# Optimization experiments

Hardware: AMD Instinct MI355X
Metric: run time of the kernel (lower is better)

## Reference

```python
import math
import jax, jax.numpy as jnp
import numpy as np
from jax import lax

LEAKY_SLOPE = 0.2
ACT_GAIN = math.sqrt(2.0)

def bilinear_filter():
    h = jnp.array([1.0, 3.0, 3.0, 1.0], dtype=jnp.float32)
    h = h[:, None] * h[None, :]
    return h / jnp.sum(h)

def setup_inputs() -> dict:
    key = jax.random.key(0)
    ks = jax.random.split(key, 6)
    B, Cin, Cout, W_DIM, R = 16, 512, 512, 512, 64
    return {
        "x": jax.random.normal(ks[0], (B, Cin, R // 2, R // 2), dtype=jnp.float32),
        "w": jax.random.normal(ks[1], (B, W_DIM), dtype=jnp.float32),
        "noise_raw": jax.random.normal(ks[2], (B, 1, R, R), dtype=jnp.float32),
        "affine_weight": jax.random.normal(ks[3], (Cin, W_DIM), dtype=jnp.float32),
        "affine_bias": jnp.ones((Cin,), dtype=jnp.float32),
        "weight": jax.random.normal(ks[4], (Cout, Cin, 3, 3), dtype=jnp.float32),
        "bias": 0.1 * jax.random.normal(ks[5], (Cout,), dtype=jnp.float32),
        "noise_strength": jnp.float32(1.0),
    }

def reference(x, w, noise_raw, affine_weight, affine_bias, weight, bias, noise_strength):
    B, Cin = x.shape[0], x.shape[1]
    Cout = weight.shape[0]
    w_dim = affine_weight.shape[1]
    # EqualizedLinear affine: weight_gain = 1/sqrt(in), bias_gain = 1, no activation
    styles = w @ (affine_weight * (1.0 / math.sqrt(w_dim))).T + affine_bias  # [B, Cin]
    # demodulation coefficients from modulated weights
    wmod = weight[None] * styles[:, None, :, None, None]                      # [B,Cout,Cin,3,3]
    dcoefs = lax.rsqrt(jnp.sum(jnp.square(wmod), axis=(2, 3, 4)) + 1e-8)     # [B, Cout]
    # modulate input instead of weights
    xs = x * styles[:, :, None, None]
    # up=True path: conv_transpose2d(x, weight.transpose(0,1), stride=2, padding=0)
    # == dilated conv with spatially flipped kernel, pad k-1=2
    w_flip = weight[:, :, ::-1, ::-1]
    y = lax.conv_general_dilated(
        xs, w_flip, window_strides=(1, 1), padding=[(2, 2), (2, 2)],
        lhs_dilation=(2, 2), dimension_numbers=("NCHW", "OIHW", "NCHW"))    # [B,Cout,2H+1,2H+1]
    # filter2d with 4x4 bilinear kernel, gain=4, padding=1 (depthwise)
    f = bilinear_filter() * 4.0
    kd = jnp.tile(f[None, None], (Cout, 1, 1, 1))                            # [Cout,1,4,4]
    y = lax.conv_general_dilated(
        y, kd, window_strides=(1, 1), padding=[(1, 1), (1, 1)],
        dimension_numbers=("NCHW", "OIHW", "NCHW"), feature_group_count=Cout)  # [B,Cout,2H,2H]
    # addcmul: noise + y * dcoefs
    noise = noise_raw * noise_strength
    y = noise + y * dcoefs[:, :, None, None]
    # bias, act gain sqrt(2), leaky relu 0.2
    y = (y + bias[None, :, None, None]) * ACT_GAIN
    return jnp.where(y >= 0, y, LEAKY_SLOPE * y)
```

## Files before the change

### kernel.cpp

```cpp
#include <hip/hip_runtime.h>
#include <hip/hip_bf16.h>
#include <stdint.h>

typedef float f32x4 __attribute__((ext_vector_type(4)));
typedef __bf16 bf16x8 __attribute__((ext_vector_type(8)));

#define GLDS16(gp, lp) __builtin_amdgcn_global_load_lds( \
    (const __attribute__((address_space(1))) void*)(gp), \
    (__attribute__((address_space(3))) void*)(lp), 16, 0, 0)

static __device__ __forceinline__ unsigned short f2bf(float f) {
    unsigned int u = __float_as_uint(f);
    u = (u + 0x7fffu + ((u >> 16) & 1u)) >> 16;
    return (unsigned short)u;
}
static __device__ __forceinline__ float bf2f(unsigned short v) {
    return __uint_as_float(((unsigned int)v) << 16);
}

#define O_STYLES 0
#define O_DCOEF  32768
#define O_XS     65536
#define O_WP     19005440
#define O_Y1     23724032
#define O_WSQ    23724032
#define WS_NEED  96075776
#define SP 1104

__global__ __launch_bounds__(256) void k_prepA(const float* __restrict__ w,
                                               const float* __restrict__ aw,
                                               const float* __restrict__ ab,
                                               const float* __restrict__ weight,
                                               float* __restrict__ styles,
                                               float* __restrict__ wsq,
                                               unsigned short* __restrict__ wp) {
    int bid = blockIdx.x;
    if (bid < 32) {
        int g = bid * 256 + threadIdx.x;
        int b = g >> 9, ci = g & 511;
        const float4* wr = (const float4*)(w + b * 512);
        const float4* ar = (const float4*)(aw + ci * 512);
        float acc = 0.f;
        for (int k = 0; k < 128; ++k) {
            float4 wv = wr[k], av = ar[k];
            acc += wv.x * av.x + wv.y * av.y + wv.z * av.z + wv.w * av.w;
        }
        styles[g] = acc * 0.04419417382415922f + ab[ci];
    } else {
        int g = (bid - 32) * 256 + threadIdx.x;
        const float* wb = weight + (long)g * 9;
        float v[9]; float s = 0.f;
#pragma unroll
        for (int t = 0; t < 9; ++t) { v[t] = wb[t]; s += v[t] * v[t]; }
        wsq[g] = s;
        const int wri[9] = {2, 2, 0, 0, 2, 0, 1, 1, 1};
        const int wci[9] = {2, 0, 2, 0, 1, 1, 2, 0, 1};
#pragma unroll
        for (int t = 0; t < 9; ++t)
            wp[t * 262144 + g] = f2bf(v[wri[t] * 3 + wci[t]]);
    }
}

__global__ __launch_bounds__(256) void k_prepB(const float* __restrict__ styles,
                                               const float* __restrict__ wsq,
                                               const float* __restrict__ x,
                                               float* __restrict__ dcoefs,
                                               unsigned short* __restrict__ xs) {
    __shared__ float T[128][33];
    int bid = blockIdx.x;
    int t = threadIdx.x;
    if (bid < 32) {
        int g = bid * 256 + t;
        int b = g >> 9, co = g & 511;
        const float4* sr = (const float4*)(styles + b * 512);
        const float4* qr = (const float4*)(wsq + co * 512);
        float acc = 1e-8f;
        for (int k = 0; k < 128; ++k) {
            float4 sv = sr[k], qv = qr[k];
            acc += sv.x * sv.x * qv.x + sv.y * sv.y * qv.y + sv.z * sv.z * qv.z + sv.w * sv.w * qv.w;
        }
        dcoefs[g] = rsqrtf(acc);
        return;
    }
    int xb = bid - 32;
    int cc = xb & 3, i = (xb >> 2) & 31, b = xb >> 7;
    int ci0 = cc * 128;
    int j4 = (t & 7) * 4, cl_r = t >> 3;
    const float* xp = x + (((long)(b * 512 + ci0)) * 32 + i) * 32;
#pragma unroll
    for (int it = 0; it < 4; ++it) {
        int cl = cl_r + it * 32;
        float4 v = *(const float4*)(xp + cl * 1024 + j4);
        T[cl][j4] = v.x; T[cl][j4 + 1] = v.y; T[cl][j4 + 2] = v.z; T[cl][j4 + 3] = v.w;
    }
    __syncthreads();
    int ci_w = t & 127, jg = t >> 7;
    float sv = styles[b * 512 + ci0 + ci_w];
    unsigned short* op = xs + (((long)(b * 34 + (i + 1))) * 34 + 1) * 512 + ci0 + ci_w;
#pragma unroll
    for (int jj = 0; jj < 16; ++jj) {
        int j = jg * 16 + jj;
        op[(long)j * 512] = f2bf(T[ci_w][j] * sv);
    }
}

#define ST_A(kk) { GLDS16(xsB + sA0 + akt + (kk)*64, smp + nb + (kk)*16384 + t16); \
                   GLDS16(xsB + sA1 + akt + (kk)*64, smp + nb + (kk)*16384 + t16 + 8192); }
#define ST_B(kk) { GLDS16(wpB + sB0 + bkt + (kk)*64, smp + nb + 32768 + (kk)*16384 + t16); \
                   GLDS16(wpB + sB1 + bkt + (kk)*64, smp + nb + 32768 + (kk)*16384 + t16 + 8192); }
#define PHASE2(kk, STG, TAILBAR) { \
  _Pragma("unroll") for (int i = 0; i < 8; ++i) \
    av[i] = *(const bf16x8*)(smp + cb + (kk)*16384 + abase + (i*16)*64); \
  _Pragma("unroll") for (int j = 0; j < 4; ++j) \
    bv[j] = *(const bf16x8*)(smp + cb + (kk)*16384 + bbase + (j*16)*64); \
  STG; \
  __builtin_amdgcn_sched_barrier(0); \
  asm volatile("s_waitcnt vmcnt(4)" ::: "memory"); \
  __builtin_amdgcn_s_barrier(); \
  asm volatile("s_waitcnt lgkmcnt(0)" ::: "memory"); \
  __builtin_amdgcn_sched_barrier(0); \
  __builtin_amdgcn_s_setprio(1); \
  _Pragma("unroll") for (int i = 0; i < 8; ++i) \
    _Pragma("unroll") for (int j = 0; j < 4; ++j) \
      acc[i][j] = __builtin_amdgcn_mfma_f32_16x16x32_bf16(av[i], bv[j], acc[i][j], 0, 0, 0); \
  __builtin_amdgcn_s_setprio(0); \
  if (TAILBAR) __builtin_amdgcn_s_barrier(); }

__global__ __launch_bounds__(512, 2) void k_conv(const unsigned short* __restrict__ xs,
                                                 const unsigned short* __restrict__ wp,
                                                 unsigned short* __restrict__ y1) {
    extern __shared__ __align__(16) char smem[];
    const unsigned char* xsB = (const unsigned char*)xs;
    const unsigned char* wpB = (const unsigned char*)wp;
    char* smp = smem;

    int d = blockIdx.x;
    int pr, nt;
    if (d >= 544) { int r = d - 544; pr = 272 + (r & 3); nt = r >> 2; }
    else          { pr = (d >> 4) * 8 + (d & 7); nt = (d >> 3) & 1; }
    int par = pr / 69;
    int Mtile = pr - par * 69;
    int Ntile = nt;
    int a_par = par >> 1, c_par = par & 1;
    int ntaps = a_par ? (c_par ? 1 : 2) : (c_par ? 2 : 4);
    int tapofs = (par == 0) ? 0 : ((par == 1) ? 4 : ((par == 2) ? 6 : 8));
    int NKT = ntaps << 3;

    int tid = threadIdx.x;
    int lane = tid & 63, wave = tid >> 6;
    int wm = wave >> 2, wn = wave & 3;
    int lrow = lane & 15;
    int rchunk = (((lane >> 4) ^ ((lrow >> 1) & 3)) << 4);
    int abase = (wm * 128 + lrow) * 64 + rchunk;
    int bbase = 32768 + (wn * 64 + lrow) * 64 + rchunk;

    int srow = tid >> 2;
    int schunk = (((tid & 3) ^ ((tid >> 3) & 3)) << 4);
    int sA0, sA1;
    {
        unsigned gm = (unsigned)(Mtile * 256 + srow);
        if (gm > 17471u) gm = 17471u;
        unsigned b_ = gm / 1092u; unsigned pix = gm - b_ * 1092u;
        unsigned r = pix / 33u; unsigned s = pix - r * 33u;
        sA0 = (int)(((b_ * 34u + r) * 34u + s) << 10) + schunk;
        gm = (unsigned)(Mtile * 256 + srow + 128);
        if (gm > 17471u) gm = 17471u;
        b_ = gm / 1092u; pix = gm - b_ * 1092u;
        r = pix / 33u; s = pix - r * 33u;
        sA1 = (int)(((b_ * 34u + r) * 34u + s) << 10) + schunk;
    }
    int sB0 = ((Ntile * 256 + srow) << 10) + schunk;
    int sB1 = sB0 + (128 << 10);
    int t16 = tid << 4;

    f32x4 acc[8][4];
#pragma unroll
    for (int i = 0; i < 8; ++i)
#pragma unroll
        for (int j = 0; j < 4; ++j)
            acc[i][j] = (f32x4){0.f, 0.f, 0.f, 0.f};
    bf16x8 av[8], bv[4];

    auto mkA = [&](int kt) -> int {
        int tl = kt >> 3; if (tl >= ntaps) tl = ntaps - 1;
        int cib = kt & 7;
        int dio = a_par ? 1 : (c_par ? tl : (tl >> 1));
        int djo = c_par ? 1 : (a_par ? tl : (tl & 1));
        return dio * 34816 + djo * 1024 + cib * 128;
    };
    auto mkB = [&](int kt) -> long {
        int tl = kt >> 3; if (tl >= ntaps) tl = ntaps - 1;
        return (long)(tapofs + tl) * 524288 + (long)((kt & 7) * 128);
    };

    {
        int akt = mkA(0); long bkt = mkB(0); int nb = 0;
        ST_A(0); ST_B(0); ST_A(1); ST_B(1);
    }
    __builtin_amdgcn_sched_barrier(0);
    asm volatile("s_waitcnt vmcnt(4)" ::: "memory");
    __builtin_amdgcn_s_barrier();

    int cur = 0;
    for (int kt = 0; kt < NKT; ++kt) {
        int akt = mkA(kt + 1);
        long bkt = mkB(kt + 1);
        int nb = (cur ^ 1) << 16;
        int cb = cur << 16;
        PHASE2(0, { ST_A(0); ST_B(0); }, 0)
        PHASE2(1, { ST_A(1); ST_B(1); }, 1)
        cur ^= 1;
    }

#pragma unroll
    for (int mf = 0; mf < 8; ++mf) {
        int gm0 = Mtile * 256 + wm * 128 + mf * 16 + ((lane >> 4) << 2);
        if (gm0 < 17472) {
            unsigned ug = (unsigned)gm0;
            unsigned bb = ug / 1092u;
            int pix0 = (int)(ug - bb * 1092u);
            long rowb = ((long)((bb * 4u + par) * 512)) * SP;
#pragma unroll
            for (int nf = 0; nf < 4; ++nf) {
                int co = Ntile * 256 + wn * 64 + nf * 16 + lrow;
                unsigned short* dst = y1 + rowb + (long)co * SP + pix0;
                if (pix0 <= 1084) {
                    ushort4 pk;
                    pk.x = f2bf(acc[mf][nf][0]);
                    pk.y = f2bf(acc[mf][nf][1]);
                    pk.z = f2bf(acc[mf][nf][2]);
                    pk.w = f2bf(acc[mf][nf][3]);
                    *(ushort4*)dst = pk;
                } else if (pix0 == 1088) {
                    dst[0] = f2bf(acc[mf][nf][0]);
                }
            }
        }
    }
}

__global__ __launch_bounds__(256) void k_blur(const unsigned short* __restrict__ y1,
                                              const float* __restrict__ dcoefs,
                                              const float* __restrict__ bias,
                                              const float* __restrict__ noise,
                                              const float* __restrict__ nstr,
                                              float* __restrict__ out) {
    __shared__ float yl[4 * 1092];
    int bid = blockIdx.x;
    int cg = bid & 127, b = bid >> 7;
    int t = threadIdx.x;
    int n = t & 63, mq = t >> 6;
    float ns = nstr[0];

    const float* npb = noise + b * 4096;

    int o = n & 1;
    int se = n >> 1;
    int sp_ = se - 1 + o;
    float a0 = o ? 1.f : 3.f;
    float a1 = o ? 3.f : 1.f;

    for (int cc = 0; cc < 4; ++cc) {
        int co = cg * 4 + cc;
#pragma unroll
        for (int pl = 0; pl < 4; ++pl) {
            const unsigned short* src = y1 + ((long)((b * 4 + pl) * 512 + co)) * SP;
            float* dst = yl + pl * 1092;
            for (int it = t; it < 273; it += 256) {
                int p0 = it * 4;
                ushort4 v = *(const ushort4*)(src + p0);
                f32x4 fv;
                fv[0] = bf2f(v.x); fv[1] = bf2f(v.y);
                fv[2] = bf2f(v.z); fv[3] = bf2f(v.w);
                *(f32x4*)(dst + p0) = fv;
            }
        }
        __syncthreads();

        float dc = dcoefs[b * 512 + co];
        float bi = bias[co];
        float* ob = out + ((long)(b * 512 + co)) * 4096;

        auto H = [&](int ap, int r) -> float {
            if ((unsigned)r > 32u) return 0.f;
            const float* pe = yl + (ap * 2) * 1092 + r * 33;
            const float* po = pe + 1092;
            float pov = (sp_ >= 0) ? po[sp_] : 0.f;
            return a0 * pe[se] + a1 * pe[se + 1] + a1 * pov + a0 * po[sp_ + 1];
        };

        int m0 = mq * 16;
        int re = m0 >> 1;
        float he0 = H(0, re), he1 = H(0, re + 1);
        float ho0 = H(1, re - 1), ho1 = H(1, re);
#pragma unroll
        for (int k = 0; k < 16; k += 2) {
            int m = m0 + k;
            float ve = 3.f * he0 + he1 + ho0 + 3.f * ho1;
            float val = npb[m * 64 + n] * ns + ve * (0.0625f * dc);
            val = (val + bi) * 1.41421356237309515f;
            ob[m * 64 + n] = (val >= 0.f) ? val : 0.2f * val;
            float hn_o = H(1, re + 1);
            float vo = he0 + 3.f * he1 + 3.f * ho1 + hn_o;
            val = npb[(m + 1) * 64 + n] * ns + vo * (0.0625f * dc);
            val = (val + bi) * 1.41421356237309515f;
            ob[(m + 1) * 64 + n] = (val >= 0.f) ? val : 0.2f * val;
            ho0 = ho1; ho1 = hn_o;
            float hn_e = H(0, re + 2);
            he0 = he1; he1 = hn_e;
            re += 1;
        }
        __syncthreads();
    }
}

extern "C" void kernel_launch(void* const* d_in, const int* in_sizes, int n_in,
                              void* d_out, int out_size, void* d_ws, size_t ws_size,
                              hipStream_t stream) {
    (void)in_sizes; (void)n_in; (void)out_size;
    if (ws_size < (size_t)WS_NEED) return;
    const float* x      = (const float*)d_in[0];
    const float* w      = (const float*)d_in[1];
    const float* noise  = (const float*)d_in[2];
    const float* aw     = (const float*)d_in[3];
    const float* ab     = (const float*)d_in[4];
    const float* weight = (const float*)d_in[5];
    const float* bias   = (const float*)d_in[6];
    const float* nstr   = (const float*)d_in[7];
    float* out = (float*)d_out;
    char* ws = (char*)d_ws;
    float* styles          = (float*)(ws + O_STYLES);
    float* dcoefs          = (float*)(ws + O_DCOEF);
    unsigned short* xs     = (unsigned short*)(ws + O_XS);
    unsigned short* wp     = (unsigned short*)(ws + O_WP);
    unsigned short* y1     = (unsigned short*)(ws + O_Y1);
    float* wsq             = (float*)(ws + O_WSQ);

    hipFuncSetAttribute((const void*)k_conv,
                        hipFuncAttributeMaxDynamicSharedMemorySize, 131072);

    hipMemsetAsync(xs, 0, 18939904, stream);
    k_prepA<<<1056, 256, 0, stream>>>(w, aw, ab, weight, styles, wsq, wp);
    k_prepB<<<2080, 256, 0, stream>>>(styles, wsq, x, dcoefs, xs);
    k_conv <<<552,  512, 131072, stream>>>(xs, wp, y1);
    k_blur <<<2048, 256, 0, stream>>>(y1, dcoefs, bias, noise, nstr, out);
}
```

Measured before the change: 192.3 us.

## Shrink conv GEMM tiles to 128x128 with 256 threads and zero only padding borders

The implicit-GEMM conv kernel moves from 256x256 tiles with 512 threads and 128KB LDS to 128x128 tiles with 256 threads and 64KB LDS. That raises the grid from 552 to 2192 blocks, which should spread work more evenly across CUs and cut the tail-wave imbalance. The full memset of the padded xs buffer is replaced by extra prepA blocks that zero only the border rows and columns, saving write bandwidth. The smaller tiles trade away operand reuse per block, so global and LDS traffic per FLOP goes up.

```diff
diff --git a/kernel.cpp b/kernel.cpp
--- a/kernel.cpp
+++ b/kernel.cpp
@@ -33,10 +33,12 @@
                                                const float* __restrict__ weight,
                                                float* __restrict__ styles,
                                                float* __restrict__ wsq,
-                                               unsigned short* __restrict__ wp) {
+                                               unsigned short* __restrict__ wp,
+                                               unsigned short* __restrict__ xs) {
     int bid = blockIdx.x;
+    int t = threadIdx.x;
     if (bid < 32) {
-        int g = bid * 256 + threadIdx.x;
+        int g = bid * 256 + t;
         int b = g >> 9, ci = g & 511;
         const float4* wr = (const float4*)(w + b * 512);
         const float4* ar = (const float4*)(aw + ci * 512);
@@ -46,18 +48,31 @@
             acc += wv.x * av.x + wv.y * av.y + wv.z * av.z + wv.w * av.w;
         }
         styles[g] = acc * 0.04419417382415922f + ab[ci];
-    } else {
-        int g = (bid - 32) * 256 + threadIdx.x;
+    } else if (bid < 1056) {
+        int g = (bid - 32) * 256 + t;
         const float* wb = weight + (long)g * 9;
         float v[9]; float s = 0.f;
 #pragma unroll
-        for (int t = 0; t < 9; ++t) { v[t] = wb[t]; s += v[t] * v[t]; }
+        for (int q = 0; q < 9; ++q) { v[q] = wb[q]; s += v[q] * v[q]; }
         wsq[g] = s;
         const int wri[9] = {2, 2, 0, 0, 2, 0, 1, 1, 1};
         const int wci[9] = {2, 0, 2, 0, 1, 1, 2, 0, 1};
 #pragma unroll
-        for (int t = 0; t < 9; ++t)
-            wp[t * 262144 + g] = f2bf(v[wri[t] * 3 + wci[t]]);
+        for (int q = 0; q < 9; ++q)
+            wp[q * 262144 + g] = f2bf(v[wri[q] * 3 + wci[q]]);
+    } else {
+        int b = bid - 1056;
+        for (int it = 0; it < 66; ++it) {
+            int idx = t + it * 256;
+            int pos = idx >> 7, q = idx & 127;
+            int r, c;
+            if (pos < 34)       { r = 0;         c = pos; }
+            else if (pos < 68)  { r = 33;        c = pos - 34; }
+            else if (pos < 100) { r = pos - 67;  c = 0; }
+            else                { r = pos - 99;  c = 33; }
+            ushort4 z = {0, 0, 0, 0};
+            *(ushort4*)(xs + (((long)(b * 34 + r)) * 34 + c) * 512 + q * 4) = z;
+        }
     }
 }
 
@@ -104,15 +119,15 @@
     }
 }
 
-#define ST_A(kk) { GLDS16(xsB + sA0 + akt + (kk)*64, smp + nb + (kk)*16384 + t16); \
-                   GLDS16(xsB + sA1 + akt + (kk)*64, smp + nb + (kk)*16384 + t16 + 8192); }
-#define ST_B(kk) { GLDS16(wpB + sB0 + bkt + (kk)*64, smp + nb + 32768 + (kk)*16384 + t16); \
-                   GLDS16(wpB + sB1 + bkt + (kk)*64, smp + nb + 32768 + (kk)*16384 + t16 + 8192); }
+#define ST_A(kk) { GLDS16(xsB + sA0 + akt + (kk)*64, smp + nb + (kk)*8192 + t16); \
+                   GLDS16(xsB + sA1 + akt + (kk)*64, smp + nb + (kk)*8192 + t16 + 4096); }
+#define ST_B(kk) { GLDS16(wpB + sB0 + bkt + (kk)*64, smp + nb + 16384 + (kk)*8192 + t16); \
+                   GLDS16(wpB + sB1 + bkt + (kk)*64, smp + nb + 16384 + (kk)*8192 + t16 + 4096); }
 #define PHASE2(kk, STG, TAILBAR) { \
-  _Pragma("unroll") for (int i = 0; i < 8; ++i) \
-    av[i] = *(const bf16x8*)(smp + cb + (kk)*16384 + abase + (i*16)*64); \
+  _Pragma("unroll") for (int i = 0; i < 4; ++i) \
+    av[i] = *(const bf16x8*)(smp + cb + (kk)*8192 + abase + (i*16)*64); \
   _Pragma("unroll") for (int j = 0; j < 4; ++j) \
-    bv[j] = *(const bf16x8*)(smp + cb + (kk)*16384 + bbase + (j*16)*64); \
+    bv[j] = *(const bf16x8*)(smp + cb + 16384 + (kk)*8192 + bbase + (j*16)*64); \
   STG; \
   __builtin_amdgcn_sched_barrier(0); \
   asm volatile("s_waitcnt vmcnt(4)" ::: "memory"); \
@@ -120,27 +135,27 @@
   asm volatile("s_waitcnt lgkmcnt(0)" ::: "memory"); \
   __builtin_amdgcn_sched_barrier(0); \
   __builtin_amdgcn_s_setprio(1); \
-  _Pragma("unroll") for (int i = 0; i < 8; ++i) \
+  _Pragma("unroll") for (int i = 0; i < 4; ++i) \
     _Pragma("unroll") for (int j = 0; j < 4; ++j) \
       acc[i][j] = __builtin_amdgcn_mfma_f32_16x16x32_bf16(av[i], bv[j], acc[i][j], 0, 0, 0); \
   __builtin_amdgcn_s_setprio(0); \
   if (TAILBAR) __builtin_amdgcn_s_barrier(); }
 
-__global__ __launch_bounds__(512, 2) void k_conv(const unsigned short* __restrict__ xs,
-                                                 const unsigned short* __restrict__ wp,
-                                                 unsigned short* __restrict__ y1) {
+__global__ __launch_bounds__(256) void k_conv(const unsigned short* __restrict__ xs,
+                                              const unsigned short* __restrict__ wp,
+                                              unsigned short* __restrict__ y1) {
     extern __shared__ __align__(16) char smem[];
     const unsigned char* xsB = (const unsigned char*)xs;
     const unsigned char* wpB = (const unsigned char*)wp;
     char* smp = smem;
 
     int d = blockIdx.x;
-    int pr, nt;
-    if (d >= 544) { int r = d - 544; pr = 272 + (r & 3); nt = r >> 2; }
-    else          { pr = (d >> 4) * 8 + (d & 7); nt = (d >> 3) & 1; }
-    int par = pr / 69;
-    int Mtile = pr - par * 69;
-    int Ntile = nt;
+    int j, nt2;
+    if (d < 2176) { int g = d >> 5, r = d & 31; j = g * 8 + (r & 7); nt2 = r >> 3; }
+    else          { int r = d - 2176; j = 544 + (r & 3); nt2 = r >> 2; }
+    int par = j / 137;
+    int Mtile = j - par * 137;
+    int Ntile = nt2;
     int a_par = par >> 1, c_par = par & 1;
     int ntaps = a_par ? (c_par ? 1 : 2) : (c_par ? 2 : 4);
     int tapofs = (par == 0) ? 0 : ((par == 1) ? 4 : ((par == 2) ? 6 : 8));
@@ -148,38 +163,38 @@
 
     int tid = threadIdx.x;
     int lane = tid & 63, wave = tid >> 6;
-    int wm = wave >> 2, wn = wave & 3;
+    int wm = wave >> 1, wn = wave & 1;
     int lrow = lane & 15;
     int rchunk = (((lane >> 4) ^ ((lrow >> 1) & 3)) << 4);
-    int abase = (wm * 128 + lrow) * 64 + rchunk;
-    int bbase = 32768 + (wn * 64 + lrow) * 64 + rchunk;
+    int abase = (wm * 64 + lrow) * 64 + rchunk;
+    int bbase = (wn * 64 + lrow) * 64 + rchunk;
 
     int srow = tid >> 2;
     int schunk = (((tid & 3) ^ ((tid >> 3) & 3)) << 4);
     int sA0, sA1;
     {
-        unsigned gm = (unsigned)(Mtile * 256 + srow);
+        unsigned gm = (unsigned)(Mtile * 128 + srow);
         if (gm > 17471u) gm = 17471u;
         unsigned b_ = gm / 1092u; unsigned pix = gm - b_ * 1092u;
         unsigned r = pix / 33u; unsigned s = pix - r * 33u;
         sA0 = (int)(((b_ * 34u + r) * 34u + s) << 10) + schunk;
-        gm = (unsigned)(Mtile * 256 + srow + 128);
+        gm = (unsigned)(Mtile * 128 + srow + 64);
         if (gm > 17471u) gm = 17471u;
         b_ = gm / 1092u; pix = gm - b_ * 1092u;
         r = pix / 33u; s = pix - r * 33u;
         sA1 = (int)(((b_ * 34u + r) * 34u + s) << 10) + schunk;
     }
-    int sB0 = ((Ntile * 256 + srow) << 10) + schunk;
-    int sB1 = sB0 + (128 << 10);
+    int sB0 = ((Ntile * 128 + srow) << 10) + schunk;
+    int sB1 = sB0 + (64 << 10);
     int t16 = tid << 4;
 
-    f32x4 acc[8][4];
-#pragma unroll
-    for (int i = 0; i < 8; ++i)
-#pragma unroll
-        for (int j = 0; j < 4; ++j)
-            acc[i][j] = (f32x4){0.f, 0.f, 0.f, 0.f};
-    bf16x8 av[8], bv[4];
+    f32x4 acc[4][4];
+#pragma unroll
+    for (int i = 0; i < 4; ++i)
+#pragma unroll
+        for (int j2 = 0; j2 < 4; ++j2)
+            acc[i][j2] = (f32x4){0.f, 0.f, 0.f, 0.f};
+    bf16x8 av[4], bv[4];
 
     auto mkA = [&](int kt) -> int {
         int tl = kt >> 3; if (tl >= ntaps) tl = ntaps - 1;
@@ -205,16 +220,17 @@
     for (int kt = 0; kt < NKT; ++kt) {
         int akt = mkA(kt + 1);
         long bkt = mkB(kt + 1);
-        int nb = (cur ^ 1) << 16;
-        int cb = cur << 16;
+        int nb = (cur ^ 1) << 15;
+        int cb = cur << 15;
         PHASE2(0, { ST_A(0); ST_B(0); }, 0)
         PHASE2(1, { ST_A(1); ST_B(1); }, 1)
         cur ^= 1;
     }
-
-#pragma unroll
-    for (int mf = 0; mf < 8; ++mf) {
-        int gm0 = Mtile * 256 + wm * 128 + mf * 16 + ((lane >> 4) << 2);
+    asm volatile("s_waitcnt vmcnt(0)" ::: "memory");
+
+#pragma unroll
+    for (int mf = 0; mf < 4; ++mf) {
+        int gm0 = Mtile * 128 + wm * 64 + mf * 16 + ((lane >> 4) << 2);
         if (gm0 < 17472) {
             unsigned ug = (unsigned)gm0;
             unsigned bb = ug / 1092u;
@@ -222,7 +238,7 @@
             long rowb = ((long)((bb * 4u + par) * 512)) * SP;
 #pragma unroll
             for (int nf = 0; nf < 4; ++nf) {
-                int co = Ntile * 256 + wn * 64 + nf * 16 + lrow;
+                int co = Ntile * 128 + wn * 64 + nf * 16 + lrow;
                 unsigned short* dst = y1 + rowb + (long)co * SP + pix0;
                 if (pix0 <= 1084) {
                     ushort4 pk;
@@ -337,11 +353,10 @@
     float* wsq             = (float*)(ws + O_WSQ);
 
     hipFuncSetAttribute((const void*)k_conv,
-                        hipFuncAttributeMaxDynamicSharedMemorySize, 131072);
-
-    hipMemsetAsync(xs, 0, 18939904, stream);
-    k_prepA<<<1056, 256, 0, stream>>>(w, aw, ab, weight, styles, wsq, wp);
+                        hipFuncAttributeMaxDynamicSharedMemorySize, 65536);
+
+    k_prepA<<<1072, 256, 0, stream>>>(w, aw, ab, weight, styles, wsq, wp, xs);
     k_prepB<<<2080, 256, 0, stream>>>(styles, wsq, x, dcoefs, xs);
-    k_conv <<<552,  512, 131072, stream>>>(xs, wp, y1);
+    k_conv <<<2192, 256, 65536, stream>>>(xs, wp, y1);
     k_blur <<<2048, 256, 0, stream>>>(y1, dcoefs, bias, noise, nstr, out);
 }
```

New measurement: 198.0 us. 1.03x slower.
